# Kernel tuning notes

Hardware: AMD Instinct MI355X
Metric: run time of the kernel (lower is better)

The kernel has to match this reference:

```python
import jax, jax.numpy as jnp
import numpy as np

N, C, H, W = 4, 256, 60, 60
CIMG = 5  # rgb/ir channels after add_position (3 + x + y)
K = 8
ITERS = 2


def setup_inputs() -> dict:
    key = jax.random.key(0)
    ks = jax.random.split(key, 12)
    inp = {
        "cnn_encoder_output": jax.random.normal(ks[0], (N, C, H, W), jnp.float32),
        "rgb": jax.random.normal(ks[1], (N, CIMG, H, W), jnp.float32),
        "ir": jax.random.normal(ks[2], (N, CIMG, H, W), jnp.float32),
        # g-MLP (mlp_num_layers=1): Linear(2C -> C), torch weight layout [out, in]
        "W_g_rgb": jax.random.normal(ks[3], (C, 2 * C), jnp.float32) * 0.02,
        "b_g_rgb": jnp.zeros((C,), jnp.float32),
        "W_g_ir": jax.random.normal(ks[4], (C, 2 * C), jnp.float32) * 0.02,
        "b_g_ir": jnp.zeros((C,), jnp.float32),
        # SE block: Linear(2C -> C//16) -> ReLU -> Linear(C//16 -> C) -> Sigmoid
        "W_se1": jax.random.normal(ks[5], (C // 16, 2 * C), jnp.float32) * 0.02,
        "b_se1": jnp.zeros((C // 16,), jnp.float32),
        "W_se2": jax.random.normal(ks[6], (C, C // 16), jnp.float32) * 0.02,
        "b_se2": jnp.zeros((C,), jnp.float32),
        "gamma": jnp.ones((1,), jnp.float32),
        "gnn_iterations": ITERS,
        "k": K,
    }
    return inp


def _knn_indices(x, k):
    # x: [N, HW, D] -> indices of k nearest neighbours [N, HW, k]
    r = jnp.einsum("nid,njd->nij", x, x)          # gram matrix
    sq = jnp.einsum("nid,nid->ni", x, x)          # squared norms
    d2 = sq[:, :, None] + sq[:, None, :] - 2.0 * r
    d = jnp.sqrt(jnp.maximum(d2, 0.0))
    d = jax.lax.stop_gradient(d)
    _, idx = jax.lax.top_k(-d, k)                  # smallest distances
    return idx


def _gather(h, idx):
    # h: [N, HW, C], idx: [N, HW, K] -> [N, HW, K, C]
    return jax.vmap(lambda hn, i: hn[i])(h, idx)


def reference(cnn_encoder_output, rgb, ir, W_g_rgb, b_g_rgb, W_g_ir, b_g_ir,
              W_se1, b_se1, W_se2, b_se2, gamma, gnn_iterations, k):
    n, c, hh, ww = cnn_encoder_output.shape
    hw = hh * ww
    rgb_f = rgb.reshape(n, rgb.shape[1], hw).transpose(0, 2, 1)  # [N, HW, 5]
    ir_f = ir.reshape(n, ir.shape[1], hw).transpose(0, 2, 1)
    knn_rgb = _knn_indices(rgb_f, k)  # [N, HW, K]
    knn_ir = _knn_indices(ir_f, k)

    h = cnn_encoder_output.transpose(0, 2, 3, 1).reshape(n, hw, c)  # [N, HW, C]

    for _ in range(gnn_iterations):
        rgb_nb = _gather(h, knn_rgb)  # [N, HW, K, C]
        ir_nb = _gather(h, knn_ir)
        rgb_feat = jnp.concatenate([rgb_nb, rgb_nb - ir_nb], axis=-1)  # [N,HW,K,2C]
        ir_feat = jnp.concatenate([ir_nb, ir_nb - rgb_nb], axis=-1)
        m_rgb = jnp.max(jax.nn.relu(jnp.einsum("nhkf,cf->nhkc", rgb_feat, W_g_rgb) + b_g_rgb), axis=2)
        m_ir = jnp.max(jax.nn.relu(jnp.einsum("nhkf,cf->nhkc", ir_feat, W_g_ir) + b_g_ir), axis=2)
        cc = jnp.concatenate([m_rgb, m_ir], axis=-1).mean(axis=1, keepdims=True)  # [N,1,2C]
        se = jax.nn.sigmoid(jax.nn.relu(cc @ W_se1.T + b_se1) @ W_se2.T + b_se2)  # [N,1,C]
        h = se * h

    h = h.reshape(n, hh, ww, c).transpose(0, 3, 1, 2)
    return jax.nn.relu(gamma * h + cnn_encoder_output)
```

## Files before the change

kernel.cpp:

```cpp
#include <hip/hip_runtime.h>
#include <hip/hip_bf16.h>

#define NB 4
#define CH 256
#define HWT 3600
#define KNN 8
#define POSB 16
#define MPAD 3712

#define SSEGP 8
#define SEGC 450
#define ROWB 225

#define GEMM_BLKS 928
#define KNN_BLKS 1024
#define B_BLKS 1952

typedef __attribute__((ext_vector_type(8))) __bf16 bf16x8;
typedef __attribute__((ext_vector_type(4))) float f32x4;

__device__ inline float med3f(float a, float b, float c) {
    return __builtin_amdgcn_fmed3f(a, b, c);
}


__device__ __forceinline__ void gemm_body(int lid, int n,
                                          const __hip_bfloat16* __restrict__ Abf,
                                          const __hip_bfloat16* __restrict__ Wbf,
                                          __hip_bfloat16* __restrict__ Yall,
                                          char* smem) {
    char* sA = smem;
    char* sB = smem + 16384;
    int w = (lid & 7) * 29 + (lid >> 3);
    int m0 = (w >> 3) * 128;
    int o0 = (w & 7) * 128;
    int t = threadIdx.x;
    int lane = t & 63, wid = t >> 6;
    int wm = wid >> 1, wo = wid & 1;

    const __hip_bfloat16* Ab = Abf + (size_t)n * MPAD * CH;
    const __hip_bfloat16* Wb = Wbf + (size_t)n * 1024 * CH;

    f32x4 acc[4][4] = {};

    int srow = t >> 3;
    int sslot = t & 7;
    int swz = (sslot ^ (srow & 7)) << 4;
    int fr = lane & 15;
    int kg = lane >> 4;
    int p = lane & 7;

    uint4 av[4], bv[4];
    auto load_tile = [&](int ks) {
#pragma unroll
        for (int r = 0; r < 4; ++r) {
            int row = srow + 32 * r;
            av[r] = *(const uint4*)(Ab + ((size_t)(m0 + row)) * CH + ks * 64 + sslot * 8);
            bv[r] = *(const uint4*)(Wb + ((size_t)(o0 + row)) * CH + ks * 64 + sslot * 8);
        }
    };
    load_tile(0);

    for (int ks = 0; ks < 4; ++ks) {
        __syncthreads();
#pragma unroll
        for (int r = 0; r < 4; ++r) {
            int row = srow + 32 * r;
            *(uint4*)(sA + row * 128 + swz) = av[r];
            *(uint4*)(sB + row * 128 + swz) = bv[r];
        }
        __syncthreads();
        if (ks < 3) load_tile(ks + 1);
#pragma unroll
        for (int kk = 0; kk < 2; ++kk) {
            bf16x8 hf[4], wf[4];
            int slot = kk * 4 + kg;
            int inrow = (slot ^ p) << 4;
#pragma unroll
            for (int f = 0; f < 4; ++f) {
                hf[f] = *(const bf16x8*)(sA + (wm * 64 + f * 16 + fr) * 128 + inrow);
                wf[f] = *(const bf16x8*)(sB + (wo * 64 + f * 16 + fr) * 128 + inrow);
            }
#pragma unroll
            for (int fa = 0; fa < 4; ++fa)
#pragma unroll
                for (int fb = 0; fb < 4; ++fb)
                    acc[fa][fb] = __builtin_amdgcn_mfma_f32_16x16x32_bf16(
                        wf[fa], hf[fb], acc[fa][fb], 0, 0, 0);
        }
    }

    __syncthreads();
#pragma unroll
    for (int fa = 0; fa < 4; ++fa)
#pragma unroll
        for (int fb = 0; fb < 4; ++fb) {
            int ml = wm * 64 + fb * 16 + fr;
            int ob = (wo * 64 + fa * 16 + kg * 4) * 2;
            f32x4 v = acc[fa][fb];
            union { ushort4 u; __hip_bfloat16 h[4]; } pk;
            pk.h[0] = __float2bfloat16(v.x);
            pk.h[1] = __float2bfloat16(v.y);
            pk.h[2] = __float2bfloat16(v.z);
            pk.h[3] = __float2bfloat16(v.w);
            int swzb = (ob & ~15) ^ ((ml & 15) << 4);
            *(ushort4*)(smem + ml * 256 + swzb + (ob & 15)) = pk.u;
        }
    __syncthreads();
    __hip_bfloat16* Y = Yall + (size_t)n * HWT * 1024;
    int colb = (t & 15) * 16;
#pragma unroll
    for (int i = 0; i < 8; ++i) {
        int row = i * 16 + (t >> 4);
        int grow = m0 + row;
        if (grow < HWT) {
            uint4 v = *(const uint4*)(smem + row * 256 + (colb ^ ((row & 15) << 4)));
            *(uint4*)((char*)Y + (size_t)grow * 2048 + o0 * 2 + colb) = v;
        }
    }
}

__device__ __forceinline__ void knn_body(int kid, const float* __restrict__ xpack,
                                         unsigned* __restrict__ partial, char* smem) {
    int seg = kid & 7;
    int rb = (kid >> 3) & 15;
    int nm = kid >> 7;
    int t = threadIdx.x;
    const float* xp = xpack + (size_t)nm * HWT * 8;
    float4* xs4 = (float4*)smem;
    float2* xs2 = (float2*)(smem + SEGC * 16);
    int j0 = seg * SEGC;
    for (int i = t; i < SEGC; i += 256) {
        const float4* s = (const float4*)(xp + (size_t)(j0 + i) * 8);
        float4 a = s[0];
        float4 b = s[1];
        xs4[i] = a;
        float2 tmp; tmp.x = b.x; tmp.y = b.y;
        xs2[i] = tmp;
    }
    __syncthreads();

    int row = rb * ROWB + t;
    bool active = (t < ROWB);
    int rr = active ? row : 0;
    float4 a0 = ((const float4*)xp)[(size_t)rr * 2];
    float4 b0 = ((const float4*)xp)[(size_t)rr * 2 + 1];
    float xi0 = a0.x, xi1 = a0.y, xi2 = a0.z, xi3 = a0.w, xi4 = b0.x;
    float qi1 = b0.y + 1.0f;

    const float BIG = __uint_as_float(0x7F000000u);
    float best[8];
#pragma unroll
    for (int i = 0; i < 8; ++i) best[i] = BIG;

    unsigned jg0 = (unsigned)j0;
#pragma unroll 5
    for (int jj = 0; jj < SEGC; ++jj) {
        float4 a = xs4[jj];
        float2 b = xs2[jj];
        float dot = a.x * xi0;
        dot = fmaf(a.y, xi1, dot);
        dot = fmaf(a.z, xi2, dot);
        dot = fmaf(a.w, xi3, dot);
        dot = fmaf(b.x, xi4, dot);
        float d2 = fmaf(-2.0f, dot, b.y + qi1);
        unsigned kb = (__float_as_uint(d2) & 0xFFFFF000u) | (jg0 + jj);
        float kf = __uint_as_float(kb);
        best[7] = med3f(best[6], best[7], kf);
        best[6] = med3f(best[5], best[6], kf);
        best[5] = med3f(best[4], best[5], kf);
        best[4] = med3f(best[3], best[4], kf);
        best[3] = med3f(best[2], best[3], kf);
        best[2] = med3f(best[1], best[2], kf);
        best[1] = med3f(best[0], best[1], kf);
        best[0] = fminf(best[0], kf);
    }
    if (active) {
        unsigned* o = partial + (((size_t)(nm * SSEGP + seg)) * HWT + row) * 8;
        uint4 lo = { __float_as_uint(best[0]), __float_as_uint(best[1]),
                     __float_as_uint(best[2]), __float_as_uint(best[3]) };
        uint4 hi = { __float_as_uint(best[4]), __float_as_uint(best[5]),
                     __float_as_uint(best[6]), __float_as_uint(best[7]) };
        ((uint4*)o)[0] = lo;
        ((uint4*)o)[1] = hi;
    }
}


__global__ __launch_bounds__(256) void fusedA(const float* __restrict__ cnn,
                                              __hip_bfloat16* __restrict__ Abf,
                                              const float* __restrict__ Wg_rgb,
                                              const float* __restrict__ Wg_ir,
                                              float* __restrict__ Wcomb,
                                              float* __restrict__ g,
                                              __hip_bfloat16* __restrict__ Wbf,
                                              const float* __restrict__ rgb,
                                              const float* __restrict__ ir,
                                              float* __restrict__ xpack) {
    int bid = blockIdx.x;
    int t = threadIdx.x;
    if (bid < GEMM_BLKS) {
        __shared__ float st[64][65];
        int n = bid / 232;
        int rem = bid - n * 232;
        int k0 = (rem / 58) * 64;
        int m0 = (rem % 58) * 64;
        const float* src = cnn + (size_t)n * CH * HWT;
#pragma unroll
        for (int r = 0; r < 4; ++r) {
            int kl = r * 16 + (t >> 4);
            int ms = (t & 15) * 4;
            float4 v = {0.f, 0.f, 0.f, 0.f};
            if (m0 + ms < HWT) v = *(const float4*)(src + (size_t)(k0 + kl) * HWT + m0 + ms);
            st[ms + 0][kl] = v.x; st[ms + 1][kl] = v.y;
            st[ms + 2][kl] = v.z; st[ms + 3][kl] = v.w;
        }
        __syncthreads();
        int m = t >> 2, kg = (t & 3) * 16;
        union { uint4 u[2]; __hip_bfloat16 h[16]; } pk;
#pragma unroll
        for (int i = 0; i < 16; ++i) pk.h[i] = __float2bfloat16(st[m][kg + i]);
        __hip_bfloat16* dst = Abf + ((size_t)n * MPAD + m0 + m) * CH + k0 + kg;
        ((uint4*)dst)[0] = pk.u[0];
        ((uint4*)dst)[1] = pk.u[1];
    } else if (bid < GEMM_BLKS + 1024) {
        int e = (bid - GEMM_BLKS) * 256 + t;
        int o = e >> 8, j = e & 255;
        float v;
        if (o < 256)      v = Wg_rgb[o * 512 + j] + Wg_rgb[o * 512 + 256 + j];
        else if (o < 512) v = Wg_rgb[(o - 256) * 512 + 256 + j];
        else if (o < 768) v = Wg_ir[(o - 512) * 512 + j] + Wg_ir[(o - 512) * 512 + 256 + j];
        else              v = Wg_ir[(o - 768) * 512 + 256 + j];
        Wcomb[e] = v;
        __hip_bfloat16 h = __float2bfloat16(v);
#pragma unroll
        for (int n = 0; n < NB; ++n) Wbf[(size_t)n * 262144 + e] = h;
        if (e < NB * CH) g[e] = 1.0f;
    } else {
        int e = (bid - GEMM_BLKS - 1024) * 256 + t;
        if (e < 2 * NB * HWT) {
            int nm = e / HWT, j = e - nm * HWT;
            int mod = nm / NB, n = nm - mod * NB;
            const float* x = (mod == 0 ? rgb : ir) + (size_t)n * 5 * HWT;
            float v[5], q = 0.f;
#pragma unroll
            for (int d = 0; d < 5; ++d) { v[d] = x[d * HWT + j]; q = fmaf(v[d], v[d], q); }
            float* o = xpack + (size_t)e * 8;
#pragma unroll
            for (int d = 0; d < 5; ++d) o[d] = v[d];
            o[5] = q; o[6] = 0.f; o[7] = 0.f;
        }
    }
}

__global__ __launch_bounds__(256) void fusedB(const __hip_bfloat16* __restrict__ Abf,
                                              const __hip_bfloat16* __restrict__ Wbf,
                                              __hip_bfloat16* __restrict__ Yall,
                                              const float* __restrict__ xpack,
                                              unsigned* __restrict__ partial) {
    __shared__ char smem[32768];
    int bid = blockIdx.x;
    if (((bid & 1) == 0) && bid < 2 * GEMM_BLKS) {
        int gid = bid >> 1;
        gemm_body(gid % 232, gid / 232, Abf, Wbf, Yall, smem);
    } else {
        int kid = (bid < 2 * GEMM_BLKS) ? (bid >> 1) : (GEMM_BLKS + bid - 2 * GEMM_BLKS);
        knn_body(kid, xpack, partial, smem);
    }
}

__global__ __launch_bounds__(256) void knn_merge_zero(const unsigned* __restrict__ partial,
                                                      int* __restrict__ knn_rgb,
                                                      int* __restrict__ knn_ir,
                                                      float* __restrict__ ccsum) {
    int bid = blockIdx.x;
    if (bid >= 450) {
        int e = (bid - 450) * 256 + threadIdx.x;
        if (e < NB * 512) ccsum[e] = 0.f;
        return;
    }
    int tid = bid * 256 + threadIdx.x;
    int rid = tid >> 1, sub = tid & 1;
    int nm = rid / HWT, row = rid - nm * HWT;
    const float BIG = __uint_as_float(0x7F000000u);
    float best[8];
#pragma unroll
    for (int i = 0; i < 8; ++i) best[i] = BIG;
    for (int s = sub; s < SSEGP; s += 2) {
        const unsigned* p = partial + (((size_t)(nm * SSEGP + s)) * HWT + row) * 8;
#pragma unroll
        for (int w = 0; w < 2; ++w) {
            uint4 v = ((const uint4*)p)[w];
            unsigned vv[4] = { v.x, v.y, v.z, v.w };
#pragma unroll
            for (int e = 0; e < 4; ++e) {
                float kf = __uint_as_float(vv[e]);
                best[7] = med3f(best[6], best[7], kf);
                best[6] = med3f(best[5], best[6], kf);
                best[5] = med3f(best[4], best[5], kf);
                best[4] = med3f(best[3], best[4], kf);
                best[3] = med3f(best[2], best[3], kf);
                best[2] = med3f(best[1], best[2], kf);
                best[1] = med3f(best[0], best[1], kf);
                best[0] = fminf(best[0], kf);
            }
        }
    }
    float other[8];
#pragma unroll
    for (int i = 0; i < 8; ++i) other[i] = __shfl_xor(best[i], 1);
#pragma unroll
    for (int i = 0; i < 8; ++i) {
        float kf = other[i];
        best[7] = med3f(best[6], best[7], kf);
        best[6] = med3f(best[5], best[6], kf);
        best[5] = med3f(best[4], best[5], kf);
        best[4] = med3f(best[3], best[4], kf);
        best[3] = med3f(best[2], best[3], kf);
        best[2] = med3f(best[1], best[2], kf);
        best[1] = med3f(best[0], best[1], kf);
        best[0] = fminf(best[0], kf);
    }
    if (sub == 0) {
        int mod = nm / NB, n = nm - mod * NB;
        int* o = (mod == 0 ? knn_rgb : knn_ir) + ((size_t)n * HWT + row) * KNN;
#pragma unroll
        for (int i = 0; i < 8; ++i) o[i] = (int)(__float_as_uint(best[i]) & 0xFFFu);
    }
}

__global__ __launch_bounds__(256) void scale_w_zero(const float* __restrict__ Wcomb,
                                                    const float* __restrict__ g,
                                                    __hip_bfloat16* __restrict__ Wbf,
                                                    float* __restrict__ ccsum) {
    int bid = blockIdx.x;
    if (bid >= 512) {
        int e = (bid - 512) * 256 + threadIdx.x;
        if (e < NB * 512) ccsum[e] = 0.f;
        return;
    }
    int n = bid >> 7;
    int gid = (bid & 127) * 256 + threadIdx.x;
    int o = gid >> 5;
    int kb = (gid & 31) * 8;
    const float* w = Wcomb + o * 256 + kb;
    const float* gp = g + n * CH + kb;
    union { uint4 u; __hip_bfloat16 h[8]; } pk;
#pragma unroll
    for (int i = 0; i < 8; ++i) pk.h[i] = __float2bfloat16(w[i] * gp[i]);
    *(uint4*)(Wbf + ((size_t)n * 1024 + o) * CH + kb) = pk.u;
}

__global__ __launch_bounds__(256) void gemm_k(const __hip_bfloat16* __restrict__ Abf,
                                              const __hip_bfloat16* __restrict__ Wbf,
                                              __hip_bfloat16* __restrict__ Yall) {
    __shared__ char smem[32768];
    int gid = blockIdx.x;
    gemm_body(gid % 232, gid / 232, Abf, Wbf, Yall, smem);
}


__global__ __launch_bounds__(256) void gather_kernel(const __hip_bfloat16* __restrict__ Yall,
                                                     const int* __restrict__ knn_rgb,
                                                     const int* __restrict__ knn_ir,
                                                     const float* __restrict__ b_rgb,
                                                     const float* __restrict__ b_ir,
                                                     float* __restrict__ ccsum) {
    int lid = blockIdx.x;
    int xcd = lid & 7, sub = lid >> 3;
    int wg = (xcd < 4 ? xcd * 113 : 4 * 113 + (xcd - 4) * 112) + sub;
    int n = wg / 225;
    int hwbase = (wg - n * 225) * POSB;
    int t = threadIdx.x;
    int half = t >> 7;
    int cp = (t & 127) << 1;
    __shared__ int sidx[POSB][2][KNN];
    {
        int p = t >> 4, rem = t & 15;
        int hw = hwbase + p;
        int v;
        if (rem < 8) v = knn_rgb[((size_t)n * HWT + hw) * KNN + rem];
        else         v = knn_ir[((size_t)n * HWT + hw) * KNN + (rem - 8)];
        sidx[p][rem >> 3][rem & 7] = v;
    }
    __syncthreads();
    const float* bias = half ? b_ir : b_rgb;
    float b0 = bias[cp], b1 = bias[cp + 1];
    float acc0 = 0.f, acc1 = 0.f;
    const __hip_bfloat16* Y = Yall + (size_t)n * HWT * 1024;
    int offA = half * 512 + cp;
    int offB = half * 512 + 256 + cp;
    for (int p = 0; p < POSB; ++p) {
        float m0 = 0.f, m1 = 0.f;
#pragma unroll
        for (int k = 0; k < KNN; ++k) {
            int jA = sidx[p][half][k];
            int jB = sidx[p][half ^ 1][k];
            unsigned u1 = *(const unsigned*)(Y + (size_t)jA * 1024 + offA);
            unsigned u2 = *(const unsigned*)(Y + (size_t)jB * 1024 + offB);
            float a0 = __uint_as_float(u1 << 16);
            float a1 = __uint_as_float(u1 & 0xFFFF0000u);
            float c0 = __uint_as_float(u2 << 16);
            float c1 = __uint_as_float(u2 & 0xFFFF0000u);
            m0 = fmaxf(m0, a0 - c0 + b0);
            m1 = fmaxf(m1, a1 - c1 + b1);
        }
        acc0 += m0;
        acc1 += m1;
    }
    atomicAdd(&ccsum[n * 512 + half * 256 + cp], acc0);
    atomicAdd(&ccsum[n * 512 + half * 256 + cp + 1], acc1);
}

__global__ __launch_bounds__(256) void se_kernel(const float* __restrict__ ccsum,
                                                 const float* __restrict__ W1,
                                                 const float* __restrict__ b1,
                                                 const float* __restrict__ W2,
                                                 const float* __restrict__ b2,
                                                 float* __restrict__ g) {
    int n = blockIdx.x;
    int t = threadIdx.x;
    __shared__ float hid[16];
    __shared__ float cc[512];
    cc[t] = ccsum[n * 512 + t] * (1.0f / HWT);
    cc[256 + t] = ccsum[n * 512 + 256 + t] * (1.0f / HWT);
    __syncthreads();
    if (t < 16) {
        float s = b1[t];
        for (int j = 0; j < 512; ++j) s = fmaf(W1[t * 512 + j], cc[j], s);
        hid[t] = fmaxf(s, 0.f);
    }
    __syncthreads();
    float s = b2[t];
#pragma unroll
    for (int q = 0; q < 16; ++q) s = fmaf(W2[t * 16 + q], hid[q], s);
    float se = 1.0f / (1.0f + expf(-s));
    g[n * CH + t] *= se;
}

__global__ void final_kernel(const float* __restrict__ cnn, const float* __restrict__ g,
                             const float* __restrict__ gamma, float* __restrict__ out) {
    int t = blockIdx.x * blockDim.x + threadIdx.x;
    if (t >= NB * CH * HWT / 4) return;
    int nc = (t * 4) / HWT;
    float4 x = ((const float4*)cnn)[t];
    float s = gamma[0] * g[nc] + 1.0f;
    float4 o;
    o.x = fmaxf(s * x.x, 0.f);
    o.y = fmaxf(s * x.y, 0.f);
    o.z = fmaxf(s * x.z, 0.f);
    o.w = fmaxf(s * x.w, 0.f);
    ((float4*)out)[t] = o;
}

extern "C" void kernel_launch(void* const* d_in, const int* in_sizes, int n_in,
                              void* d_out, int out_size, void* d_ws, size_t ws_size,
                              hipStream_t stream) {
    const float* cnn    = (const float*)d_in[0];
    const float* rgb    = (const float*)d_in[1];
    const float* ir     = (const float*)d_in[2];
    const float* Wg_rgb = (const float*)d_in[3];
    const float* bg_rgb = (const float*)d_in[4];
    const float* Wg_ir  = (const float*)d_in[5];
    const float* bg_ir  = (const float*)d_in[6];
    const float* Wse1   = (const float*)d_in[7];
    const float* bse1   = (const float*)d_in[8];
    const float* Wse2   = (const float*)d_in[9];
    const float* bse2   = (const float*)d_in[10];
    const float* gamma  = (const float*)d_in[11];
    float* out = (float*)d_out;

    char* ws = (char*)d_ws;
    size_t off = 0;
    float* xpack = (float*)(ws + off); off += (size_t)2 * NB * HWT * 8 * 4;
    int* knn_rgb = (int*)(ws + off); off += (size_t)NB * HWT * KNN * 4;
    int* knn_ir  = (int*)(ws + off); off += (size_t)NB * HWT * KNN * 4;
    float* Wcomb = (float*)(ws + off); off += (size_t)1024 * 256 * 4;
    __hip_bfloat16* Wbf = (__hip_bfloat16*)(ws + off); off += (size_t)NB * 1024 * CH * 2;
    __hip_bfloat16* Abf = (__hip_bfloat16*)(ws + off); off += (size_t)NB * MPAD * CH * 2;
    __hip_bfloat16* Yall = (__hip_bfloat16*)(ws + off); off += (size_t)NB * HWT * 1024 * 2;
    unsigned* partial = (unsigned*)(ws + off);
    off += (size_t)2 * NB * SSEGP * HWT * 8 * 4;
    float* ccsum = (float*)(ws + off); off += (size_t)NB * 512 * 4;
    float* g     = (float*)(ws + off); off += (size_t)NB * CH * 4;

    fusedA<<<GEMM_BLKS + 1024 + 113, 256, 0, stream>>>(cnn, Abf, Wg_rgb, Wg_ir, Wcomb, g,
                                                       Wbf, rgb, ir, xpack);
    fusedB<<<B_BLKS, 256, 0, stream>>>(Abf, Wbf, Yall, xpack, partial);
    knn_merge_zero<<<458, 256, 0, stream>>>(partial, knn_rgb, knn_ir, ccsum);
    gather_kernel<<<900, 256, 0, stream>>>(Yall, knn_rgb, knn_ir, bg_rgb, bg_ir, ccsum);
    se_kernel<<<NB, 256, 0, stream>>>(ccsum, Wse1, bse1, Wse2, bse2, g);
    scale_w_zero<<<520, 256, 0, stream>>>(Wcomb, g, Wbf, ccsum);
    gemm_k<<<GEMM_BLKS, 256, 0, stream>>>(Abf, Wbf, Yall);
    gather_kernel<<<900, 256, 0, stream>>>(Yall, knn_rgb, knn_ir, bg_rgb, bg_ir, ccsum);
    se_kernel<<<NB, 256, 0, stream>>>(ccsum, Wse1, bse1, Wse2, bse2, g);
    final_kernel<<<3600, 256, 0, stream>>>(cnn, g, gamma, out);
}
```

Before: 231.1 us.

## Split fused GEMM/KNN kernel; register-block KNN over two rows and paired candidates

Replaces the interleaved GEMM+KNN fusedB kernel with two separate launches: a dedicated KNN kernel and the standalone GEMM. The new KNN kernel has each thread handle two query rows and reads candidate pairs from a transposed shared layout, so packed float2 math can be used and each shared load serves more work. This uses 512 blocks instead of 1024. The GEMM epilogue now writes its output with nontemporal stores. In exchange, the GEMM and KNN phases no longer overlap inside one kernel, and each thread carries more live registers.

```diff
diff --git a/kernel.cpp b/kernel.cpp
--- a/kernel.cpp
+++ b/kernel.cpp
@@ -9,18 +9,31 @@
 #define MPAD 3712
 
 #define SSEGP 8
-#define SEGC 450
-#define ROWB 225
+#define CAND 450
+#define PAIRS 225
+#define ROWS3 450
 
 #define GEMM_BLKS 928
-#define KNN_BLKS 1024
-#define B_BLKS 1952
 
 typedef __attribute__((ext_vector_type(8))) __bf16 bf16x8;
 typedef __attribute__((ext_vector_type(4))) float f32x4;
+typedef __attribute__((ext_vector_type(2))) float f32x2;
+typedef __attribute__((ext_vector_type(2))) unsigned u32x2;
+typedef __attribute__((ext_vector_type(4))) unsigned u32x4;
 
 __device__ inline float med3f(float a, float b, float c) {
     return __builtin_amdgcn_fmed3f(a, b, c);
+}
+
+__device__ __forceinline__ void insert8(float* best, float kf) {
+    best[7] = med3f(best[6], best[7], kf);
+    best[6] = med3f(best[5], best[6], kf);
+    best[5] = med3f(best[4], best[5], kf);
+    best[4] = med3f(best[3], best[4], kf);
+    best[3] = med3f(best[2], best[3], kf);
+    best[2] = med3f(best[1], best[2], kf);
+    best[1] = med3f(best[0], best[1], kf);
+    best[0] = fminf(best[0], kf);
 }
 
 
@@ -114,78 +127,105 @@
         int row = i * 16 + (t >> 4);
         int grow = m0 + row;
         if (grow < HWT) {
-            uint4 v = *(const uint4*)(smem + row * 256 + (colb ^ ((row & 15) << 4)));
-            *(uint4*)((char*)Y + (size_t)grow * 2048 + o0 * 2 + colb) = v;
-        }
-    }
-}
-
-__device__ __forceinline__ void knn_body(int kid, const float* __restrict__ xpack,
-                                         unsigned* __restrict__ partial, char* smem) {
-    int seg = kid & 7;
-    int rb = (kid >> 3) & 15;
-    int nm = kid >> 7;
+            u32x4 v = *(const u32x4*)(smem + row * 256 + (colb ^ ((row & 15) << 4)));
+            __builtin_nontemporal_store(v, (u32x4*)((char*)Y + (size_t)grow * 2048 + o0 * 2 + colb));
+        }
+    }
+}
+
+__global__ __launch_bounds__(256) void gemm_k(const __hip_bfloat16* __restrict__ Abf,
+                                              const __hip_bfloat16* __restrict__ Wbf,
+                                              __hip_bfloat16* __restrict__ Yall) {
+    __shared__ char smem[32768];
+    int gid = blockIdx.x;
+    gemm_body(gid % 232, gid / 232, Abf, Wbf, Yall, smem);
+}
+
+__global__ __launch_bounds__(256) void knn_main(const float* __restrict__ xpack,
+                                                unsigned* __restrict__ partial) {
+    int seg = blockIdx.x, rb = blockIdx.y, nm = blockIdx.z;
     int t = threadIdx.x;
     const float* xp = xpack + (size_t)nm * HWT * 8;
-    float4* xs4 = (float4*)smem;
-    float2* xs2 = (float2*)(smem + SEGC * 16);
-    int j0 = seg * SEGC;
-    for (int i = t; i < SEGC; i += 256) {
-        const float4* s = (const float4*)(xp + (size_t)(j0 + i) * 8);
-        float4 a = s[0];
-        float4 b = s[1];
-        xs4[i] = a;
-        float2 tmp; tmp.x = b.x; tmp.y = b.y;
-        xs2[i] = tmp;
-    }
-    __syncthreads();
-
-    int row = rb * ROWB + t;
-    bool active = (t < ROWB);
-    int rr = active ? row : 0;
-    float4 a0 = ((const float4*)xp)[(size_t)rr * 2];
-    float4 b0 = ((const float4*)xp)[(size_t)rr * 2 + 1];
-    float xi0 = a0.x, xi1 = a0.y, xi2 = a0.z, xi3 = a0.w, xi4 = b0.x;
-    float qi1 = b0.y + 1.0f;
+    __shared__ f32x2 xs[PAIRS * 6];
+
+    if (t < PAIRS) {
+        int j = seg * CAND + 2 * t;
+        float4 a0 = ((const float4*)xp)[(size_t)j * 2];
+        float4 b0 = ((const float4*)xp)[(size_t)j * 2 + 1];
+        float4 a1 = ((const float4*)xp)[(size_t)(j + 1) * 2];
+        float4 b1 = ((const float4*)xp)[(size_t)(j + 1) * 2 + 1];
+        f32x2* o = xs + t * 6;
+        o[0] = f32x2{a0.x, a1.x};
+        o[1] = f32x2{a0.y, a1.y};
+        o[2] = f32x2{a0.z, a1.z};
+        o[3] = f32x2{a0.w, a1.w};
+        o[4] = f32x2{b0.x, b1.x};
+        o[5] = f32x2{b0.y + 1.0f, b1.y + 1.0f};
+    }
+    __syncthreads();
+
+    bool active = (t < PAIRS);
+    int r0 = rb * ROWS3 + t;
+    int rr0 = active ? r0 : 0;
+    int rr1 = active ? (r0 + PAIRS) : 0;
+    float4 a0 = ((const float4*)xp)[(size_t)rr0 * 2];
+    float4 b0 = ((const float4*)xp)[(size_t)rr0 * 2 + 1];
+    float4 a1 = ((const float4*)xp)[(size_t)rr1 * 2];
+    float4 b1 = ((const float4*)xp)[(size_t)rr1 * 2 + 1];
+    f32x2 q01 = f32x2{b0.y, b0.y};
+    f32x2 q11 = f32x2{b1.y, b1.y};
 
     const float BIG = __uint_as_float(0x7F000000u);
-    float best[8];
-#pragma unroll
-    for (int i = 0; i < 8; ++i) best[i] = BIG;
-
-    unsigned jg0 = (unsigned)j0;
-#pragma unroll 5
-    for (int jj = 0; jj < SEGC; ++jj) {
-        float4 a = xs4[jj];
-        float2 b = xs2[jj];
-        float dot = a.x * xi0;
-        dot = fmaf(a.y, xi1, dot);
-        dot = fmaf(a.z, xi2, dot);
-        dot = fmaf(a.w, xi3, dot);
-        dot = fmaf(b.x, xi4, dot);
-        float d2 = fmaf(-2.0f, dot, b.y + qi1);
-        unsigned kb = (__float_as_uint(d2) & 0xFFFFF000u) | (jg0 + jj);
-        float kf = __uint_as_float(kb);
-        best[7] = med3f(best[6], best[7], kf);
-        best[6] = med3f(best[5], best[6], kf);
-        best[5] = med3f(best[4], best[5], kf);
-        best[4] = med3f(best[3], best[4], kf);
-        best[3] = med3f(best[2], best[3], kf);
-        best[2] = med3f(best[1], best[2], kf);
-        best[1] = med3f(best[0], best[1], kf);
-        best[0] = fminf(best[0], kf);
+    float bst0[8], bst1[8];
+#pragma unroll
+    for (int i = 0; i < 8; ++i) { bst0[i] = BIG; bst1[i] = BIG; }
+
+    unsigned jg0 = (unsigned)(seg * CAND);
+#pragma unroll 3
+    for (int p = 0; p < PAIRS; ++p) {
+        f32x2 cx = xs[p * 6 + 0];
+        f32x2 cy = xs[p * 6 + 1];
+        f32x2 cz = xs[p * 6 + 2];
+        f32x2 cw = xs[p * 6 + 3];
+        f32x2 cv = xs[p * 6 + 4];
+        f32x2 cq = xs[p * 6 + 5];
+        f32x2 d0 = cx * a0.x;
+        d0 += cy * a0.y;
+        d0 += cz * a0.z;
+        d0 += cw * a0.w;
+        d0 += cv * b0.x;
+        f32x2 s0 = cq + q01;
+        f32x2 e0 = s0 - 2.0f * d0;
+        f32x2 d1 = cx * a1.x;
+        d1 += cy * a1.y;
+        d1 += cz * a1.z;
+        d1 += cw * a1.w;
+        d1 += cv * b1.x;
+        f32x2 s1 = cq + q11;
+        f32x2 e1 = s1 - 2.0f * d1;
+
+        unsigned jA = jg0 + 2 * p, jB = jA + 1;
+        u32x2 u0, u1;
+        __builtin_memcpy(&u0, &e0, 8);
+        __builtin_memcpy(&u1, &e1, 8);
+        insert8(bst0, __uint_as_float((u0.x & 0xFFFFF000u) | jA));
+        insert8(bst0, __uint_as_float((u0.y & 0xFFFFF000u) | jB));
+        insert8(bst1, __uint_as_float((u1.x & 0xFFFFF000u) | jA));
+        insert8(bst1, __uint_as_float((u1.y & 0xFFFFF000u) | jB));
     }
     if (active) {
-        unsigned* o = partial + (((size_t)(nm * SSEGP + seg)) * HWT + row) * 8;
-        uint4 lo = { __float_as_uint(best[0]), __float_as_uint(best[1]),
-                     __float_as_uint(best[2]), __float_as_uint(best[3]) };
-        uint4 hi = { __float_as_uint(best[4]), __float_as_uint(best[5]),
-                     __float_as_uint(best[6]), __float_as_uint(best[7]) };
-        ((uint4*)o)[0] = lo;
-        ((uint4*)o)[1] = hi;
-    }
-}
-
+        unsigned* o = partial + (((size_t)(nm * SSEGP + seg)) * HWT + r0) * 8;
+        ((uint4*)o)[0] = uint4{ __float_as_uint(bst0[0]), __float_as_uint(bst0[1]),
+                                __float_as_uint(bst0[2]), __float_as_uint(bst0[3]) };
+        ((uint4*)o)[1] = uint4{ __float_as_uint(bst0[4]), __float_as_uint(bst0[5]),
+                                __float_as_uint(bst0[6]), __float_as_uint(bst0[7]) };
+        unsigned* o1 = partial + (((size_t)(nm * SSEGP + seg)) * HWT + r0 + PAIRS) * 8;
+        ((uint4*)o1)[0] = uint4{ __float_as_uint(bst1[0]), __float_as_uint(bst1[1]),
+                                 __float_as_uint(bst1[2]), __float_as_uint(bst1[3]) };
+        ((uint4*)o1)[1] = uint4{ __float_as_uint(bst1[4]), __float_as_uint(bst1[5]),
+                                 __float_as_uint(bst1[6]), __float_as_uint(bst1[7]) };
+    }
+}
 
 __global__ __launch_bounds__(256) void fusedA(const float* __restrict__ cnn,
                                               __hip_bfloat16* __restrict__ Abf,
@@ -253,22 +293,6 @@
     }
 }
 
-__global__ __launch_bounds__(256) void fusedB(const __hip_bfloat16* __restrict__ Abf,
-                                              const __hip_bfloat16* __restrict__ Wbf,
-                                              __hip_bfloat16* __restrict__ Yall,
-                                              const float* __restrict__ xpack,
-                                              unsigned* __restrict__ partial) {
-    __shared__ char smem[32768];
-    int bid = blockIdx.x;
-    if (((bid & 1) == 0) && bid < 2 * GEMM_BLKS) {
-        int gid = bid >> 1;
-        gemm_body(gid % 232, gid / 232, Abf, Wbf, Yall, smem);
-    } else {
-        int kid = (bid < 2 * GEMM_BLKS) ? (bid >> 1) : (GEMM_BLKS + bid - 2 * GEMM_BLKS);
-        knn_body(kid, xpack, partial, smem);
-    }
-}
-
 __global__ __launch_bounds__(256) void knn_merge_zero(const unsigned* __restrict__ partial,
                                                       int* __restrict__ knn_rgb,
                                                       int* __restrict__ knn_ir,
@@ -293,34 +317,14 @@
             uint4 v = ((const uint4*)p)[w];
             unsigned vv[4] = { v.x, v.y, v.z, v.w };
 #pragma unroll
-            for (int e = 0; e < 4; ++e) {
-                float kf = __uint_as_float(vv[e]);
-                best[7] = med3f(best[6], best[7], kf);
-                best[6] = med3f(best[5], best[6], kf);
-                best[5] = med3f(best[4], best[5], kf);
-                best[4] = med3f(best[3], best[4], kf);
-                best[3] = med3f(best[2], best[3], kf);
-                best[2] = med3f(best[1], best[2], kf);
-                best[1] = med3f(best[0], best[1], kf);
-                best[0] = fminf(best[0], kf);
-            }
+            for (int e = 0; e < 4; ++e) insert8(best, __uint_as_float(vv[e]));
         }
     }
     float other[8];
 #pragma unroll
     for (int i = 0; i < 8; ++i) other[i] = __shfl_xor(best[i], 1);
 #pragma unroll
-    for (int i = 0; i < 8; ++i) {
-        float kf = other[i];
-        best[7] = med3f(best[6], best[7], kf);
-        best[6] = med3f(best[5], best[6], kf);
-        best[5] = med3f(best[4], best[5], kf);
-        best[4] = med3f(best[3], best[4], kf);
-        best[3] = med3f(best[2], best[3], kf);
-        best[2] = med3f(best[1], best[2], kf);
-        best[1] = med3f(best[0], best[1], kf);
-        best[0] = fminf(best[0], kf);
-    }
+    for (int i = 0; i < 8; ++i) insert8(best, other[i]);
     if (sub == 0) {
         int mod = nm / NB, n = nm - mod * NB;
         int* o = (mod == 0 ? knn_rgb : knn_ir) + ((size_t)n * HWT + row) * KNN;
@@ -350,15 +354,6 @@
     for (int i = 0; i < 8; ++i) pk.h[i] = __float2bfloat16(w[i] * gp[i]);
     *(uint4*)(Wbf + ((size_t)n * 1024 + o) * CH + kb) = pk.u;
 }
-
-__global__ __launch_bounds__(256) void gemm_k(const __hip_bfloat16* __restrict__ Abf,
-                                              const __hip_bfloat16* __restrict__ Wbf,
-                                              __hip_bfloat16* __restrict__ Yall) {
-    __shared__ char smem[32768];
-    int gid = blockIdx.x;
-    gemm_body(gid % 232, gid / 232, Abf, Wbf, Yall, smem);
-}
-
 
 __global__ __launch_bounds__(256) void gather_kernel(const __hip_bfloat16* __restrict__ Yall,
                                                      const int* __restrict__ knn_rgb,
@@ -486,7 +481,8 @@
 
     fusedA<<<GEMM_BLKS + 1024 + 113, 256, 0, stream>>>(cnn, Abf, Wg_rgb, Wg_ir, Wcomb, g,
                                                        Wbf, rgb, ir, xpack);
-    fusedB<<<B_BLKS, 256, 0, stream>>>(Abf, Wbf, Yall, xpack, partial);
+    knn_main<<<dim3(SSEGP, 8, 2 * NB), 256, 0, stream>>>(xpack, partial);
+    gemm_k<<<GEMM_BLKS, 256, 0, stream>>>(Abf, Wbf, Yall);
     knn_merge_zero<<<458, 256, 0, stream>>>(partial, knn_rgb, knn_ir, ccsum);
     gather_kernel<<<900, 256, 0, stream>>>(Yall, knn_rgb, knn_ir, bg_rgb, bg_ir, ccsum);
     se_kernel<<<NB, 256, 0, stream>>>(ccsum, Wse1, bse1, Wse2, bse2, g);
```

Measured after the change: 239.4 us. 1.04x slower.
